# Optimization experiments

Hardware: AMD Instinct MI355X
Metric: run time of the kernel (lower is better)

The kernel has to match this reference:

```python
import jax, jax.numpy as jnp
import numpy as np


def setup_inputs() -> dict:
    key = jax.random.key(0)
    kq, kk, kv, km = jax.random.split(key, 4)
    B, H, S, D = 2, 16, 2048, 64
    queries = jax.random.normal(kq, (B, H, S, D), dtype=jnp.float32)
    keys = jax.random.normal(kk, (B, H, S, D), dtype=jnp.float32)
    values = jax.random.normal(kv, (B, H, S, D), dtype=jnp.float32)
    # additive binary mask (1 = masked position), broadcast over batch/heads
    mask = jax.random.randint(km, (1, 1, S, S), 0, 2, dtype=jnp.int32)
    return {"queries": queries, "keys": keys, "values": values,
            "mask": mask, "key_dim": D}


def reference(queries, keys, values, mask, key_dim):
    # scores = Q K^T / sqrt(d)   -> [B, H, S, S]
    scale = 1.0 / jnp.sqrt(jnp.asarray(key_dim, dtype=jnp.float32))
    scores = jnp.einsum('bhqd,bhkd->bhqk', queries, keys) * scale
    # additive mask: masked positions get -1e9
    scores = scores + (-1.0e9) * mask.astype(scores.dtype)
    weights = jax.nn.softmax(scores, axis=-1)
    # attention output: weights @ V -> [B, H, S, D]
    return jnp.einsum('bhqk,bhkd->bhqd', weights, values)
```

## Files before the change

kernel.cpp:

```cpp
#include <hip/hip_runtime.h>

typedef __attribute__((ext_vector_type(8))) short short8;
typedef __attribute__((ext_vector_type(4))) float floatx4;
typedef __attribute__((ext_vector_type(4))) unsigned short ushort4v;

#define S_LEN 2048
#define D_HEAD 64
#define NT64 (S_LEN / 64)
#define PITCH 72
#define TP 73
#define SCALE2 0.18033688f
#define MASK_BIAS2 -2.0e9f

static __device__ __forceinline__ unsigned short f2bf(float f) {
  unsigned int x = __builtin_bit_cast(unsigned int, f);
  x += 0x7fffu + ((x >> 16) & 1u);
  return (unsigned short)(x >> 16);
}
static __device__ __forceinline__ float bf2f(unsigned short u) {
  unsigned int x = ((unsigned int)u) << 16;
  return __builtin_bit_cast(float, x);
}
static __device__ __forceinline__ short8 cvt8(const float* __restrict__ p) {
  float4 a = *(const float4*)p;
  float4 b = *(const float4*)(p + 4);
  short8 r;
  r[0] = (short)f2bf(a.x); r[1] = (short)f2bf(a.y);
  r[2] = (short)f2bf(a.z); r[3] = (short)f2bf(a.w);
  r[4] = (short)f2bf(b.x); r[5] = (short)f2bf(b.y);
  r[6] = (short)f2bf(b.z); r[7] = (short)f2bf(b.w);
  return r;
}
static __device__ __forceinline__ short8 cvt8s(const float* __restrict__ p) {
  float4 a = *(const float4*)p;
  float4 b = *(const float4*)(p + 4);
  short8 r;
  r[0] = (short)f2bf(a.x * SCALE2); r[1] = (short)f2bf(a.y * SCALE2);
  r[2] = (short)f2bf(a.z * SCALE2); r[3] = (short)f2bf(a.w * SCALE2);
  r[4] = (short)f2bf(b.x * SCALE2); r[5] = (short)f2bf(b.y * SCALE2);
  r[6] = (short)f2bf(b.z * SCALE2); r[7] = (short)f2bf(b.w * SCALE2);
  return r;
}
static __device__ __forceinline__ void cp16(const void* g, void* l) {
  __builtin_amdgcn_global_load_lds(
      (const __attribute__((address_space(1))) unsigned int*)g,
      (__attribute__((address_space(3))) unsigned int*)l, 16, 0, 0);
}
static __device__ __forceinline__ unsigned int pk2f(float a, float b) {
  const unsigned int ab = __builtin_bit_cast(unsigned int, a) + 0x8000u;
  const unsigned int bb = __builtin_bit_cast(unsigned int, b) + 0x8000u;
  return __builtin_amdgcn_perm(bb, ab, 0x07060302u);
}

__global__ __launch_bounds__(256) void prep(
    const float* __restrict__ K, const float* __restrict__ V,
    const int* __restrict__ mask,
    unsigned short* __restrict__ Kws, unsigned short* __restrict__ Vws,
    unsigned long long* __restrict__ Mb, int BH)
{
  __shared__ unsigned short t[D_HEAD * TP];
  const int tid = threadIdx.x;
  const int nbK = BH * 64;
  const int nbV = BH * 32;
  int b = blockIdx.x;

  if (b < nbK) {
    const int tt   = b * 256 + tid;
    const int bh   = tt >> 14;
    const int rem  = tt & 16383;
    const int tile = rem >> 9;
    const int n    = rem & 511;
    const int row  = n >> 3;
    const int col8 = (n & 7) ^ (row & 7);
    short8 r = cvt8(K + ((size_t)(bh * S_LEN + tile * 64 + row)) * D_HEAD + col8 * 8);
    *(short8*)(Kws + (size_t)tt * 8) = r;
    return;
  }
  b -= nbK;
  if (b < nbV) {
    const int tile = b & 31;
    const int bh   = b >> 5;
    const int s0   = tile * 64;
    const float* Vb = V + (size_t)bh * S_LEN * D_HEAD;
#pragma unroll
    for (int p = 0; p < 4; ++p) {
      const int s  = p * 16 + (tid >> 4);
      const int d0 = (tid & 15) * 4;
      float4 v = *(const float4*)(Vb + (size_t)(s0 + s) * D_HEAD + d0);
      unsigned short* dst = &t[s * TP + d0];
      dst[0] = f2bf(v.x); dst[1] = f2bf(v.y); dst[2] = f2bf(v.z); dst[3] = f2bf(v.w);
    }
    __syncthreads();
    unsigned short* Vo = Vws + ((size_t)(bh * 32 + tile)) * 4096;
#pragma unroll
    for (int p = 0; p < 2; ++p) {
      const int n    = p * 256 + tid;
      const int d    = n >> 3;
      const int col8 = (n & 7) ^ (d & 7);
      short8 r;
#pragma unroll
      for (int j = 0; j < 8; ++j) r[j] = (short)t[(col8 * 8 + j) * TP + d];
      *(short8*)(Vo + (size_t)n * 8) = r;
    }
    return;
  }
  b -= nbV;
  const int rg   = b >> 2;
  const int cq   = b & 3;
  const int lane = tid & 63;
  const int row  = rg * 4 + (tid >> 6);
#pragma unroll 8
  for (int c = cq * 8; c < cq * 8 + 8; ++c) {
    const int mv = mask[(size_t)row * S_LEN + c * 64 + lane];
    const unsigned long long bm = __ballot(mv != 0);
    if (lane == 0) Mb[(size_t)row * NT64 + c] = bm;
  }
}

__global__ __launch_bounds__(256, 2) void fa_fwd9(
    const float* __restrict__ Q,
    const unsigned short* __restrict__ Kws,
    const unsigned short* __restrict__ Vws,
    const unsigned long long* __restrict__ Mb,
    float* __restrict__ Out)
{
  __shared__ unsigned short Kbuf[3][64 * 64];
  __shared__ unsigned short Vbuf[3][64 * 64];
  __shared__ unsigned short Plds[4][32 * 64];

  const int tid  = threadIdx.x;
  const int wv   = tid >> 6;
  const int lane = tid & 63;
  const int quad = lane >> 4;
  const int l16  = lane & 15;
  const int l8   = l16 & 7;

  const int nwg  = gridDim.x;
  const int flat = blockIdx.x;
  const int swz  = (flat & 7) * (nwg >> 3) + (flat >> 3);
  const int bh   = swz >> 4;
  const int qw   = (swz & 15) * 128 + wv * 32;

  const float* Qb = Q + (size_t)bh * S_LEN * D_HEAD;
  const unsigned short* KT = Kws + (size_t)bh * NT64 * 4096;
  const unsigned short* VT = Vws + (size_t)bh * NT64 * 4096;

  auto stage = [&](int kt, int buf) {
#pragma unroll
    for (int j = 0; j < 2; ++j) {
      const int c0 = (wv * 2 + j) * 64;
      cp16(KT + (size_t)kt * 4096 + (size_t)(c0 + lane) * 8, &Kbuf[buf][c0 * 8]);
      cp16(VT + (size_t)kt * 4096 + (size_t)(c0 + lane) * 8, &Vbuf[buf][c0 * 8]);
    }
  };

  stage(0, 0);
  stage(1, 1);

  short8 qfrag[2][2];
#pragma unroll
  for (int g = 0; g < 2; ++g)
#pragma unroll
    for (int w = 0; w < 2; ++w)
      qfrag[g][w] = cvt8s(Qb + (size_t)(qw + g * 16 + l16) * D_HEAD + w * 32 + quad * 8);

  short8 kones;
#pragma unroll
  for (int j = 0; j < 8; ++j) kones[j] = (short)0x3F80;

  floatx4 ot[2][4];
#pragma unroll
  for (int g = 0; g < 2; ++g)
#pragma unroll
    for (int dt = 0; dt < 4; ++dt) ot[g][dt] = (floatx4){0.f, 0.f, 0.f, 0.f};
  floatx4 lacc[2];
  lacc[0] = (floatx4){0.f, 0.f, 0.f, 0.f};
  lacc[1] = (floatx4){0.f, 0.f, 0.f, 0.f};

  unsigned short* pl = &Plds[wv][0];
  const unsigned long long* mrowp[2];
#pragma unroll
  for (int g = 0; g < 2; ++g)
    mrowp[g] = Mb + (size_t)(qw + g * 16 + l16) * NT64;

  asm volatile("s_waitcnt vmcnt(4)" ::: "memory");
  __builtin_amdgcn_s_barrier();

  int cur = 0;
  for (int kt = 0; kt < NT64; ++kt) {
    const int sb = cur == 0 ? 2 : cur - 1;
    if (kt + 2 < NT64) stage(kt + 2, sb);
    const unsigned short* Kl = Kbuf[cur];
    const unsigned short* Vl = Vbuf[cur];

    floatx4 st[2][4];
#pragma unroll
    for (int g = 0; g < 2; ++g)
#pragma unroll
      for (int nt = 0; nt < 4; ++nt) st[g][nt] = (floatx4){0.f, 0.f, 0.f, 0.f};
    __builtin_amdgcn_s_setprio(1);
#pragma unroll
    for (int w = 0; w < 2; ++w)
#pragma unroll
      for (int nt = 0; nt < 4; ++nt) {
        short8 kf = *(const short8*)&Kl[(nt * 16 + l16) * 64 + (((w * 4 + quad) ^ l8) * 8)];
        st[0][nt] = __builtin_amdgcn_mfma_f32_16x16x32_bf16(kf, qfrag[0][w], st[0][nt], 0, 0, 0);
        st[1][nt] = __builtin_amdgcn_mfma_f32_16x16x32_bf16(kf, qfrag[1][w], st[1][nt], 0, 0, 0);
      }
    __builtin_amdgcn_s_setprio(0);

#pragma unroll
    for (int g = 0; g < 2; ++g) {
      const unsigned long long mw = mrowp[g][kt];
#pragma unroll
      for (int nt = 0; nt < 4; ++nt) {
        const unsigned nib = (unsigned)(mw >> (nt * 16 + quad * 4)) & 0xFu;
        float p[4];
#pragma unroll
        for (int r = 0; r < 4; ++r) {
          float pv = __builtin_amdgcn_exp2f(st[g][nt][r]);
          p[r] = ((nib >> r) & 1u) ? 0.0f : pv;
        }
        const unsigned int d0 = pk2f(p[0], p[1]);
        const unsigned int d1 = pk2f(p[2], p[3]);
        const int c = nt * 2 + (quad >> 1);
        unsigned int* dst = (unsigned int*)&pl[(g * 16 + l16) * 64 + ((c ^ l8) * 8) + (quad & 1) * 4];
        dst[0] = d0; dst[1] = d1;
      }
    }

    __builtin_amdgcn_s_setprio(1);
#pragma unroll
    for (int w = 0; w < 2; ++w) {
      short8 pf0 = *(const short8*)&pl[(l16) * 64 + (((w * 4 + quad) ^ l8) * 8)];
      short8 pf1 = *(const short8*)&pl[(16 + l16) * 64 + (((w * 4 + quad) ^ l8) * 8)];
      lacc[0] = __builtin_amdgcn_mfma_f32_16x16x32_bf16(kones, pf0, lacc[0], 0, 0, 0);
      lacc[1] = __builtin_amdgcn_mfma_f32_16x16x32_bf16(kones, pf1, lacc[1], 0, 0, 0);
#pragma unroll
      for (int dt = 0; dt < 4; ++dt) {
        short8 vf = *(const short8*)&Vl[(dt * 16 + l16) * 64 + (((w * 4 + quad) ^ l8) * 8)];
        ot[0][dt] = __builtin_amdgcn_mfma_f32_16x16x32_bf16(vf, pf0, ot[0][dt], 0, 0, 0);
        ot[1][dt] = __builtin_amdgcn_mfma_f32_16x16x32_bf16(vf, pf1, ot[1][dt], 0, 0, 0);
      }
    }
    __builtin_amdgcn_s_setprio(0);

    if (kt + 2 < NT64) {
      asm volatile("s_waitcnt vmcnt(4)" ::: "memory");
      __builtin_amdgcn_s_barrier();
    } else if (kt + 1 < NT64) {
      asm volatile("s_waitcnt vmcnt(0)" ::: "memory");
      __builtin_amdgcn_s_barrier();
    }
    cur = cur == 2 ? 0 : cur + 1;
  }

#pragma unroll
  for (int g = 0; g < 2; ++g) {
    const float invl = 1.0f / lacc[g][0];
    float* Ob = Out + (size_t)bh * S_LEN * D_HEAD + (size_t)(qw + g * 16 + l16) * D_HEAD;
#pragma unroll
    for (int dt = 0; dt < 4; ++dt) {
      float4 v;
      v.x = ot[g][dt][0] * invl; v.y = ot[g][dt][1] * invl;
      v.z = ot[g][dt][2] * invl; v.w = ot[g][dt][3] * invl;
      *(float4*)(Ob + dt * 16 + quad * 4) = v;
    }
  }
}

__global__ __launch_bounds__(256) void fa_fwd(
    const float* __restrict__ Q, const float* __restrict__ K, const float* __restrict__ V,
    const int* __restrict__ mask, float* __restrict__ Out)
{
  __shared__ unsigned short Vt[D_HEAD * PITCH];
  __shared__ unsigned short Plds[4][16 * PITCH];
  const int tid = threadIdx.x, wv = tid >> 6, lane = tid & 63, quad = lane >> 4, l16 = lane & 15;
  const int bh = blockIdx.y, qw = blockIdx.x * 64 + wv * 16;
  const float* Qb = Q + (size_t)bh * S_LEN * D_HEAD;
  const float* Kb = K + (size_t)bh * S_LEN * D_HEAD;
  const float* Vb = V + (size_t)bh * S_LEN * D_HEAD;
  short8 qfrag[2];
#pragma unroll
  for (int w = 0; w < 2; ++w)
    qfrag[w] = cvt8(Qb + (size_t)(qw + l16) * D_HEAD + w * 32 + quad * 8);
  floatx4 o[4];
#pragma unroll
  for (int nt = 0; nt < 4; ++nt) o[nt] = (floatx4){0.f, 0.f, 0.f, 0.f};
  float m_run[4], l_run[4];
#pragma unroll
  for (int r = 0; r < 4; ++r) { m_run[r] = -1.0e30f; l_run[r] = 0.f; }
  unsigned short* pl = &Plds[wv][0];
  for (int kt = 0; kt < NT64; ++kt) {
    const int k0 = kt * 64;
    __syncthreads();
#pragma unroll
    for (int it = 0; it < 2; ++it) {
      const int s = it * 32 + (tid >> 3), d0 = (tid & 7) * 8, dblk = (tid & 7);
      const int swz = (((s >> 3) ^ dblk) & 7) * 8 + (s & 7);
      const float* vp = Vb + (size_t)(k0 + s) * D_HEAD + d0;
      float4 a = *(const float4*)vp; float4 bb = *(const float4*)(vp + 4);
      const float vvv[8] = {a.x, a.y, a.z, a.w, bb.x, bb.y, bb.z, bb.w};
#pragma unroll
      for (int j = 0; j < 8; ++j) Vt[(d0 + j) * PITCH + swz] = f2bf(vvv[j]);
    }
    __syncthreads();
    floatx4 scf[4];
#pragma unroll
    for (int nt = 0; nt < 4; ++nt) scf[nt] = (floatx4){0.f, 0.f, 0.f, 0.f};
#pragma unroll
    for (int w = 0; w < 2; ++w)
#pragma unroll
      for (int nt = 0; nt < 4; ++nt) {
        short8 kf = cvt8(Kb + (size_t)(k0 + nt * 16 + l16) * D_HEAD + w * 32 + quad * 8);
        scf[nt] = __builtin_amdgcn_mfma_f32_16x16x32_bf16(qfrag[w], kf, scf[nt], 0, 0, 0);
      }
    float s_val[4][4], mloc[4] = {-1.0e30f, -1.0e30f, -1.0e30f, -1.0e30f};
#pragma unroll
    for (int nt = 0; nt < 4; ++nt)
#pragma unroll
      for (int r = 0; r < 4; ++r) {
        const int mk = mask[(size_t)(qw + quad * 4 + r) * S_LEN + (k0 + nt * 16 + l16)];
        const float sv = scf[nt][r] * SCALE2 + (mk ? MASK_BIAS2 : 0.0f);
        s_val[nt][r] = sv; mloc[r] = fmaxf(mloc[r], sv);
      }
#pragma unroll
    for (int r = 0; r < 4; ++r)
#pragma unroll
      for (int off = 1; off < 16; off <<= 1) mloc[r] = fmaxf(mloc[r], __shfl_xor(mloc[r], off));
    float alpha[4], rsum[4];
#pragma unroll
    for (int r = 0; r < 4; ++r) {
      const float mnew = fmaxf(m_run[r], mloc[r]);
      alpha[r] = exp2f(m_run[r] - mnew); m_run[r] = mnew; rsum[r] = 0.f;
    }
#pragma unroll
    for (int nt = 0; nt < 4; ++nt)
#pragma unroll
      for (int r = 0; r < 4; ++r) {
        const float p = exp2f(s_val[nt][r] - m_run[r]);
        const unsigned short ph = f2bf(p);
        rsum[r] += bf2f(ph);
        pl[(quad * 4 + r) * PITCH + nt * 16 + l16] = ph;
      }
    __syncthreads();
#pragma unroll
    for (int r = 0; r < 4; ++r) {
#pragma unroll
      for (int off = 1; off < 16; off <<= 1) rsum[r] += __shfl_xor(rsum[r], off);
      l_run[r] = l_run[r] * alpha[r] + rsum[r];
    }
#pragma unroll
    for (int nt = 0; nt < 4; ++nt)
#pragma unroll
      for (int r = 0; r < 4; ++r) o[nt][r] *= alpha[r];
#pragma unroll
    for (int w = 0; w < 2; ++w) {
      short8 af = *(const short8*)&pl[l16 * PITCH + w * 32 + quad * 8];
#pragma unroll
      for (int nt = 0; nt < 4; ++nt) {
        const int d = nt * 16 + l16, blk = ((w * 4 + quad) ^ (d >> 3)) & 7;
        short8 vf = *(const short8*)&Vt[d * PITCH + blk * 8];
        o[nt] = __builtin_amdgcn_mfma_f32_16x16x32_bf16(af, vf, o[nt], 0, 0, 0);
      }
    }
  }
  float invl[4];
#pragma unroll
  for (int r = 0; r < 4; ++r) invl[r] = 1.0f / l_run[r];
  float* Ob = Out + (size_t)bh * S_LEN * D_HEAD;
#pragma unroll
  for (int nt = 0; nt < 4; ++nt)
#pragma unroll
    for (int r = 0; r < 4; ++r)
      Ob[(size_t)(qw + quad * 4 + r) * D_HEAD + nt * 16 + l16] = o[nt][r] * invl[r];
}

extern "C" void kernel_launch(void* const* d_in, const int* in_sizes, int n_in,
                              void* d_out, int out_size, void* d_ws, size_t ws_size,
                              hipStream_t stream) {
  const float* Q = (const float*)d_in[0];
  const float* K = (const float*)d_in[1];
  const float* V = (const float*)d_in[2];
  const int* mask = (const int*)d_in[3];
  float* Out = (float*)d_out;
  const int BH = in_sizes[0] / (S_LEN * D_HEAD);
  const size_t NH = (size_t)BH * S_LEN * D_HEAD;
  const size_t nMb = (size_t)S_LEN * NT64;
  const size_t need = NH * 2 * 2 + nMb * 8;

  if (ws_size >= need) {
    unsigned short* Kws = (unsigned short*)d_ws;
    unsigned short* Vws = Kws + NH;
    unsigned long long* Mbits = (unsigned long long*)(Vws + NH);
    const int nbPrep = BH * 64 + BH * 32 + S_LEN;
    prep<<<dim3(nbPrep), 256, 0, stream>>>(K, V, mask, Kws, Vws, Mbits, BH);
    fa_fwd9<<<dim3((S_LEN / 128) * BH), 256, 0, stream>>>(Q, Kws, Vws, Mbits, Out);
  } else {
    fa_fwd<<<dim3(S_LEN / 64, BH), 256, 0, stream>>>(Q, K, V, mask, Out);
  }
}
```

Measured before the change: 168.5 us.

## Keep P in registers via permlane swaps and software-pipeline QK with PV

Drops the per-wave LDS staging of the probability tile. P is now rearranged into MFMA B-operand layout directly in registers with v_permlane32_swap and v_permlane16_swap. The main loop is also software-pipelined: QK^T for tile kt+1 is issued before the softmax and PV of tile kt, using two ping-ponged score register sets. The wait before the barrier changes to vmcnt(0) at the top of each iteration. The aim is to cut LDS traffic and overlap MFMA work with exp and pack work, at the cost of more registers, which could hurt occupancy at 2 blocks per CU.

Result: no change. 170.2 us (+1.0%).

```diff
diff --git a/kernel.cpp b/kernel.cpp
--- a/kernel.cpp
+++ b/kernel.cpp
@@ -2,7 +2,7 @@
 
 typedef __attribute__((ext_vector_type(8))) short short8;
 typedef __attribute__((ext_vector_type(4))) float floatx4;
-typedef __attribute__((ext_vector_type(4))) unsigned short ushort4v;
+typedef __attribute__((ext_vector_type(2))) unsigned int uint2v;
 
 #define S_LEN 2048
 #define D_HEAD 64
@@ -50,6 +50,22 @@
   const unsigned int ab = __builtin_bit_cast(unsigned int, a) + 0x8000u;
   const unsigned int bb = __builtin_bit_cast(unsigned int, b) + 0x8000u;
   return __builtin_amdgcn_perm(bb, ab, 0x07060302u);
+}
+static __device__ __forceinline__ void plswap32(unsigned int& a, unsigned int& b) {
+#if __has_builtin(__builtin_amdgcn_permlane32_swap)
+  uint2v r = __builtin_amdgcn_permlane32_swap(a, b, false, false);
+  a = r[0]; b = r[1];
+#else
+  asm volatile("v_permlane32_swap_b32 %0, %1" : "+v"(a), "+v"(b));
+#endif
+}
+static __device__ __forceinline__ void plswap16(unsigned int& a, unsigned int& b) {
+#if __has_builtin(__builtin_amdgcn_permlane16_swap)
+  uint2v r = __builtin_amdgcn_permlane16_swap(a, b, false, false);
+  a = r[0]; b = r[1];
+#else
+  asm volatile("v_permlane16_swap_b32 %0, %1" : "+v"(a), "+v"(b));
+#endif
 }
 
 __global__ __launch_bounds__(256) void prep(
@@ -126,7 +142,6 @@
 {
   __shared__ unsigned short Kbuf[3][64 * 64];
   __shared__ unsigned short Vbuf[3][64 * 64];
-  __shared__ unsigned short Plds[4][32 * 64];
 
   const int tid  = threadIdx.x;
   const int wv   = tid >> 6;
@@ -177,83 +192,99 @@
   lacc[0] = (floatx4){0.f, 0.f, 0.f, 0.f};
   lacc[1] = (floatx4){0.f, 0.f, 0.f, 0.f};
 
-  unsigned short* pl = &Plds[wv][0];
   const unsigned long long* mrowp[2];
 #pragma unroll
   for (int g = 0; g < 2; ++g)
     mrowp[g] = Mb + (size_t)(qw + g * 16 + l16) * NT64;
 
-  asm volatile("s_waitcnt vmcnt(4)" ::: "memory");
-  __builtin_amdgcn_s_barrier();
-
-  int cur = 0;
-  for (int kt = 0; kt < NT64; ++kt) {
-    const int sb = cur == 0 ? 2 : cur - 1;
-    if (kt + 2 < NT64) stage(kt + 2, sb);
-    const unsigned short* Kl = Kbuf[cur];
-    const unsigned short* Vl = Vbuf[cur];
-
-    floatx4 st[2][4];
+  floatx4 stA[2][4], stB[2][4];
+
+  auto qk = [&](floatx4 (&sdst)[2][4], const unsigned short* Kl) {
 #pragma unroll
     for (int g = 0; g < 2; ++g)
 #pragma unroll
-      for (int nt = 0; nt < 4; ++nt) st[g][nt] = (floatx4){0.f, 0.f, 0.f, 0.f};
+      for (int nt = 0; nt < 4; ++nt) sdst[g][nt] = (floatx4){0.f, 0.f, 0.f, 0.f};
     __builtin_amdgcn_s_setprio(1);
 #pragma unroll
     for (int w = 0; w < 2; ++w)
 #pragma unroll
       for (int nt = 0; nt < 4; ++nt) {
         short8 kf = *(const short8*)&Kl[(nt * 16 + l16) * 64 + (((w * 4 + quad) ^ l8) * 8)];
-        st[0][nt] = __builtin_amdgcn_mfma_f32_16x16x32_bf16(kf, qfrag[0][w], st[0][nt], 0, 0, 0);
-        st[1][nt] = __builtin_amdgcn_mfma_f32_16x16x32_bf16(kf, qfrag[1][w], st[1][nt], 0, 0, 0);
+        sdst[0][nt] = __builtin_amdgcn_mfma_f32_16x16x32_bf16(kf, qfrag[0][w], sdst[0][nt], 0, 0, 0);
+        sdst[1][nt] = __builtin_amdgcn_mfma_f32_16x16x32_bf16(kf, qfrag[1][w], sdst[1][nt], 0, 0, 0);
       }
     __builtin_amdgcn_s_setprio(0);
-
+  };
+
+  auto sm_pv = [&](floatx4 (&scur)[2][4], const int kt, const unsigned short* Vl) {
+    short8 pf[2][2];
 #pragma unroll
     for (int g = 0; g < 2; ++g) {
       const unsigned long long mw = mrowp[g][kt];
+      unsigned int Wk[4][2];
 #pragma unroll
       for (int nt = 0; nt < 4; ++nt) {
         const unsigned nib = (unsigned)(mw >> (nt * 16 + quad * 4)) & 0xFu;
         float p[4];
 #pragma unroll
         for (int r = 0; r < 4; ++r) {
-          float pv = __builtin_amdgcn_exp2f(st[g][nt][r]);
+          float pv = __builtin_amdgcn_exp2f(scur[g][nt][r]);
           p[r] = ((nib >> r) & 1u) ? 0.0f : pv;
         }
-        const unsigned int d0 = pk2f(p[0], p[1]);
-        const unsigned int d1 = pk2f(p[2], p[3]);
-        const int c = nt * 2 + (quad >> 1);
-        unsigned int* dst = (unsigned int*)&pl[(g * 16 + l16) * 64 + ((c ^ l8) * 8) + (quad & 1) * 4];
-        dst[0] = d0; dst[1] = d1;
-      }
-    }
-
+        Wk[nt][0] = pk2f(p[0], p[1]);
+        Wk[nt][1] = pk2f(p[2], p[3]);
+      }
+#pragma unroll
+      for (int w = 0; w < 2; ++w) {
+        unsigned a0 = Wk[2 * w][0], b0 = Wk[2 * w + 1][0];
+        plswap32(a0, b0);
+        plswap16(a0, b0);
+        unsigned a1 = Wk[2 * w][1], b1 = Wk[2 * w + 1][1];
+        plswap32(a1, b1);
+        plswap16(a1, b1);
+        uint4 wd;
+        wd.x = a0; wd.y = a1; wd.z = b0; wd.w = b1;
+        pf[g][w] = __builtin_bit_cast(short8, wd);
+      }
+    }
     __builtin_amdgcn_s_setprio(1);
 #pragma unroll
     for (int w = 0; w < 2; ++w) {
-      short8 pf0 = *(const short8*)&pl[(l16) * 64 + (((w * 4 + quad) ^ l8) * 8)];
-      short8 pf1 = *(const short8*)&pl[(16 + l16) * 64 + (((w * 4 + quad) ^ l8) * 8)];
-      lacc[0] = __builtin_amdgcn_mfma_f32_16x16x32_bf16(kones, pf0, lacc[0], 0, 0, 0);
-      lacc[1] = __builtin_amdgcn_mfma_f32_16x16x32_bf16(kones, pf1, lacc[1], 0, 0, 0);
+      lacc[0] = __builtin_amdgcn_mfma_f32_16x16x32_bf16(kones, pf[0][w], lacc[0], 0, 0, 0);
+      lacc[1] = __builtin_amdgcn_mfma_f32_16x16x32_bf16(kones, pf[1][w], lacc[1], 0, 0, 0);
 #pragma unroll
       for (int dt = 0; dt < 4; ++dt) {
         short8 vf = *(const short8*)&Vl[(dt * 16 + l16) * 64 + (((w * 4 + quad) ^ l8) * 8)];
-        ot[0][dt] = __builtin_amdgcn_mfma_f32_16x16x32_bf16(vf, pf0, ot[0][dt], 0, 0, 0);
-        ot[1][dt] = __builtin_amdgcn_mfma_f32_16x16x32_bf16(vf, pf1, ot[1][dt], 0, 0, 0);
+        ot[0][dt] = __builtin_amdgcn_mfma_f32_16x16x32_bf16(vf, pf[0][w], ot[0][dt], 0, 0, 0);
+        ot[1][dt] = __builtin_amdgcn_mfma_f32_16x16x32_bf16(vf, pf[1][w], ot[1][dt], 0, 0, 0);
       }
     }
     __builtin_amdgcn_s_setprio(0);
-
-    if (kt + 2 < NT64) {
-      asm volatile("s_waitcnt vmcnt(4)" ::: "memory");
-      __builtin_amdgcn_s_barrier();
-    } else if (kt + 1 < NT64) {
-      asm volatile("s_waitcnt vmcnt(0)" ::: "memory");
-      __builtin_amdgcn_s_barrier();
-    }
-    cur = cur == 2 ? 0 : cur + 1;
-  }
+  };
+
+  auto body = [&](floatx4 (&scur)[2][4], floatx4 (&snxt)[2][4],
+                  const int kt, const int bV, const int bKn, const int bS) {
+    asm volatile("s_waitcnt vmcnt(0)" ::: "memory");
+    __builtin_amdgcn_s_barrier();
+    if (kt + 2 < NT64) stage(kt + 2, bS);
+    qk(snxt, Kbuf[bKn]);
+    sm_pv(scur, kt, Vbuf[bV]);
+  };
+
+  asm volatile("s_waitcnt vmcnt(0)" ::: "memory");
+  __builtin_amdgcn_s_barrier();
+  qk(stA, Kbuf[0]);
+
+  int bV = 0, bKn = 1, bS = 2;
+  for (int kt = 0; kt < NT64 - 2; kt += 2) {
+    body(stA, stB, kt, bV, bKn, bS);
+    { const int t = bV; bV = bKn; bKn = bS; bS = t; }
+    body(stB, stA, kt + 1, bV, bKn, bS);
+    { const int t = bV; bV = bKn; bKn = bS; bS = t; }
+  }
+  body(stA, stB, NT64 - 2, bV, bKn, bS);
+  { const int t = bV; bV = bKn; bKn = bS; bS = t; }
+  sm_pv(stB, NT64 - 1, Vbuf[bV]);
 
 #pragma unroll
   for (int g = 0; g < 2; ++g) {
```
